# Optimization experiments

Hardware: AMD Instinct MI355X
Metric: run time of the kernel (lower is better)

The kernel has to match this reference:

```python
import jax, jax.numpy as jnp
from jax import lax
import numpy as np

WIN = 9  # default window [9, 9] in the original module


def _box_sum(x, win):
    """Sum over a win x win window, stride 1, pad win//2 (same as conv2d with ones kernel).
    Implemented separably (two 1D convs) - mathematically identical to the 2D ones-kernel conv.
    x: [B, 1, H, W] float32.
    """
    pad = win // 2
    kh = jnp.ones((1, 1, win, 1), x.dtype)
    kw = jnp.ones((1, 1, 1, win), x.dtype)
    dn = lax.conv_dimension_numbers(x.shape, kh.shape, ('NCHW', 'OIHW', 'NCHW'))
    y = lax.conv_general_dilated(x, kh, (1, 1), [(pad, pad), (0, 0)], dimension_numbers=dn)
    return lax.conv_general_dilated(y, kw, (1, 1), [(0, 0), (pad, pad)], dimension_numbers=dn)


def setup_inputs() -> dict:
    key = jax.random.key(0)
    k1, k2 = jax.random.split(key)
    shape = (32, 1, 512, 512)
    predict = jax.random.uniform(k1, shape, dtype=jnp.float32)
    target = jax.random.uniform(k2, shape, dtype=jnp.float32)
    return {"predict": predict, "target": target}


def reference(predict, target):
    win = WIN
    win_size = jnp.asarray(win * win, jnp.float32)

    I, J = predict, target
    I_sum = _box_sum(I, win)
    J_sum = _box_sum(J, win)
    I2_sum = _box_sum(I * I, win)
    J2_sum = _box_sum(J * J, win)
    IJ_sum = _box_sum(I * J, win)

    u_I = I_sum / win_size
    u_J = J_sum / win_size

    cross = IJ_sum - u_J * I_sum - u_I * J_sum + u_I * u_J * win_size
    I_var = I2_sum - 2.0 * u_I * I_sum + u_I * u_I * win_size
    J_var = J2_sum - 2.0 * u_J * J_sum + u_J * u_J * win_size

    cc = cross * cross / (I_var * J_var + 1e-6)
    return -jnp.mean(cc) + 1.0
```

## Files before the change

### kernel.cpp

```cpp
#include <hip/hip_runtime.h>


#define W 512
#define H 512
#define BH 16
#define NBANDS (H / BH)
#define NTHREADS 128

__device__ __forceinline__ float4 ld4(const float* p) {
    return *reinterpret_cast<const float4*>(p);
}

template<bool ADD>
__device__ __forceinline__ void row_accum(const float* __restrict__ Ip,
                                          const float* __restrict__ Jp,
                                          int rowbase, int x0,
                                          float vs[5][4]) {
    const float4 zz = make_float4(0.f, 0.f, 0.f, 0.f);
    float4 a0 = (x0 >= 4)     ? ld4(Ip + rowbase + x0 - 4) : zz;
    float4 a1 =                 ld4(Ip + rowbase + x0);
    float4 a2 = (x0 <= W - 8) ? ld4(Ip + rowbase + x0 + 4) : zz;
    float4 b0 = (x0 >= 4)     ? ld4(Jp + rowbase + x0 - 4) : zz;
    float4 b1 =                 ld4(Jp + rowbase + x0);
    float4 b2 = (x0 <= W - 8) ? ld4(Jp + rowbase + x0 + 4) : zz;

    float iv[12], jv[12];
    iv[0]=a0.x; iv[1]=a0.y; iv[2]=a0.z; iv[3]=a0.w;
    iv[4]=a1.x; iv[5]=a1.y; iv[6]=a1.z; iv[7]=a1.w;
    iv[8]=a2.x; iv[9]=a2.y; iv[10]=a2.z; iv[11]=a2.w;
    jv[0]=b0.x; jv[1]=b0.y; jv[2]=b0.z; jv[3]=b0.w;
    jv[4]=b1.x; jv[5]=b1.y; jv[6]=b1.z; jv[7]=b1.w;
    jv[8]=b2.x; jv[9]=b2.y; jv[10]=b2.z; jv[11]=b2.w;

    auto doq = [&](int qi, auto f) {
        float p[12];
        #pragma unroll
        for (int k = 0; k < 12; ++k) p[k] = f(k);
        float t = p[0];
        #pragma unroll
        for (int k = 1; k < 9; ++k) t += p[k];
        if (ADD) vs[qi][0] += t; else vs[qi][0] -= t;
        #pragma unroll
        for (int c = 1; c < 4; ++c) {
            t += p[c + 8] - p[c - 1];
            if (ADD) vs[qi][c] += t; else vs[qi][c] -= t;
        }
    };
    doq(0, [&](int k) { return iv[k]; });
    doq(1, [&](int k) { return jv[k]; });
    doq(2, [&](int k) { return iv[k] * iv[k]; });
    doq(3, [&](int k) { return jv[k] * jv[k]; });
    doq(4, [&](int k) { return iv[k] * jv[k]; });
}

__global__ __launch_bounds__(NTHREADS)
void ncc_main(const float* __restrict__ I, const float* __restrict__ J,
              float* __restrict__ partials) {
    const int blk  = blockIdx.x;
    const int b    = blk / NBANDS;
    const int band = blk % NBANDS;
    const int y0   = band * BH;
    const float* Ip = I + (size_t)b * (H * W);
    const float* Jp = J + (size_t)b * (H * W);
    const int x0 = (int)threadIdx.x * 4;

    float vs[5][4];
    #pragma unroll
    for (int q = 0; q < 5; ++q)
        #pragma unroll
        for (int c = 0; c < 4; ++c) vs[q][c] = 0.f;

    #pragma unroll
    for (int dr = -4; dr < 4; ++dr) {
        int r = y0 + dr;
        if (r >= 0 && r < H) row_accum<true>(Ip, Jp, r * W, x0, vs);
    }

    float cc_acc = 0.f;
    const float inv81 = 1.f / 81.f;
    for (int y = y0; y < y0 + BH; ++y) {
        int ra = y + 4;
        if (ra < H) row_accum<true>(Ip, Jp, ra * W, x0, vs);
        #pragma unroll
        for (int c = 0; c < 4; ++c) {
            float Is = vs[0][c], Js = vs[1][c];
            float I2 = vs[2][c], J2 = vs[3][c], IJ = vs[4][c];
            float cross = IJ - Is * Js * inv81;
            float Ivar  = I2 - Is * Is * inv81;
            float Jvar  = J2 - Js * Js * inv81;
            cc_acc += cross * cross / (Ivar * Jvar + 1e-6f);
        }
        int rs = y - 4;
        if (rs >= 0) row_accum<false>(Ip, Jp, rs * W, x0, vs);
    }

    #pragma unroll
    for (int off = 32; off > 0; off >>= 1)
        cc_acc += __shfl_down(cc_acc, off, 64);
    __shared__ float wsum[NTHREADS / 64];
    if ((threadIdx.x & 63) == 0) wsum[threadIdx.x >> 6] = cc_acc;
    __syncthreads();
    if (threadIdx.x == 0) partials[blockIdx.x] = wsum[0] + wsum[1];
}

__global__ __launch_bounds__(256)
void ncc_finish(const float* __restrict__ partials, float* __restrict__ out,
                int n, float inv_total) {
    float v = 0.f;
    for (int i = threadIdx.x; i < n; i += blockDim.x) v += partials[i];
    #pragma unroll
    for (int off = 32; off > 0; off >>= 1)
        v += __shfl_down(v, off, 64);
    __shared__ float wsum[4];
    if ((threadIdx.x & 63) == 0) wsum[threadIdx.x >> 6] = v;
    __syncthreads();
    if (threadIdx.x == 0) {
        float t = wsum[0] + wsum[1] + wsum[2] + wsum[3];
        out[0] = 1.0f - t * inv_total;
    }
}

extern "C" void kernel_launch(void* const* d_in, const int* in_sizes, int n_in,
                              void* d_out, int out_size, void* d_ws, size_t ws_size,
                              hipStream_t stream) {
    const float* I = (const float*)d_in[0];
    const float* J = (const float*)d_in[1];
    float* out = (float*)d_out;
    float* partials = (float*)d_ws;

    const int n = in_sizes[0];
    const int B = n / (H * W);
    const int nblocks = B * NBANDS;

    ncc_main<<<nblocks, NTHREADS, 0, stream>>>(I, J, partials);
    ncc_finish<<<1, 256, 0, stream>>>(partials, out, nblocks, 1.0f / (float)n);
}
```

Baseline: 119.6 us.

## Rewrite NCC kernel with register row ring, wave shuffles for horizontal sums

Each thread now owns two columns with 256 threads per block. It keeps a register ring of prefetched row pairs and does the vertical running sum first, then forms horizontal 9-wide sums through cross-lane shuffles, with wave-edge halos exchanged via double-buffered shared memory. Blocks are remapped with an XCD-style swizzle, and division is replaced by a hardware reciprocal. This removes the redundant 12-wide horizontal loads and the per-row recomputation. In exchange it adds a block barrier per row pair, shared-memory traffic and approximate reciprocal precision.

```diff
diff --git a/kernel.cpp b/kernel.cpp
--- a/kernel.cpp
+++ b/kernel.cpp
@@ -5,102 +5,161 @@
 #define H 512
 #define BH 16
 #define NBANDS (H / BH)
-#define NTHREADS 128
+#define NT 256
 
-__device__ __forceinline__ float4 ld4(const float* p) {
-    return *reinterpret_cast<const float4*>(p);
-}
-
-template<bool ADD>
-__device__ __forceinline__ void row_accum(const float* __restrict__ Ip,
-                                          const float* __restrict__ Jp,
-                                          int rowbase, int x0,
-                                          float vs[5][4]) {
-    const float4 zz = make_float4(0.f, 0.f, 0.f, 0.f);
-    float4 a0 = (x0 >= 4)     ? ld4(Ip + rowbase + x0 - 4) : zz;
-    float4 a1 =                 ld4(Ip + rowbase + x0);
-    float4 a2 = (x0 <= W - 8) ? ld4(Ip + rowbase + x0 + 4) : zz;
-    float4 b0 = (x0 >= 4)     ? ld4(Jp + rowbase + x0 - 4) : zz;
-    float4 b1 =                 ld4(Jp + rowbase + x0);
-    float4 b2 = (x0 <= W - 8) ? ld4(Jp + rowbase + x0 + 4) : zz;
-
-    float iv[12], jv[12];
-    iv[0]=a0.x; iv[1]=a0.y; iv[2]=a0.z; iv[3]=a0.w;
-    iv[4]=a1.x; iv[5]=a1.y; iv[6]=a1.z; iv[7]=a1.w;
-    iv[8]=a2.x; iv[9]=a2.y; iv[10]=a2.z; iv[11]=a2.w;
-    jv[0]=b0.x; jv[1]=b0.y; jv[2]=b0.z; jv[3]=b0.w;
-    jv[4]=b1.x; jv[5]=b1.y; jv[6]=b1.z; jv[7]=b1.w;
-    jv[8]=b2.x; jv[9]=b2.y; jv[10]=b2.z; jv[11]=b2.w;
-
-    auto doq = [&](int qi, auto f) {
-        float p[12];
-        #pragma unroll
-        for (int k = 0; k < 12; ++k) p[k] = f(k);
-        float t = p[0];
-        #pragma unroll
-        for (int k = 1; k < 9; ++k) t += p[k];
-        if (ADD) vs[qi][0] += t; else vs[qi][0] -= t;
-        #pragma unroll
-        for (int c = 1; c < 4; ++c) {
-            t += p[c + 8] - p[c - 1];
-            if (ADD) vs[qi][c] += t; else vs[qi][c] -= t;
-        }
-    };
-    doq(0, [&](int k) { return iv[k]; });
-    doq(1, [&](int k) { return jv[k]; });
-    doq(2, [&](int k) { return iv[k] * iv[k]; });
-    doq(3, [&](int k) { return jv[k] * jv[k]; });
-    doq(4, [&](int k) { return iv[k] * jv[k]; });
-}
-
-__global__ __launch_bounds__(NTHREADS)
+__global__ __launch_bounds__(NT)
 void ncc_main(const float* __restrict__ I, const float* __restrict__ J,
               float* __restrict__ partials) {
-    const int blk  = blockIdx.x;
-    const int b    = blk / NBANDS;
-    const int band = blk % NBANDS;
+    __shared__ float eb[2][2][6][4][5][3];
+    __shared__ float wsum[4];
+
+    const int tid  = threadIdx.x;
+    const int lane = tid & 63;
+    const int wid  = tid >> 6;
+
+    const int nblk = gridDim.x;
+    const int g    = (blockIdx.x & 7) * (nblk >> 3) + (blockIdx.x >> 3);
+
+    const int b    = g >> 5;
+    const int band = g & (NBANDS - 1);
     const int y0   = band * BH;
     const float* Ip = I + (size_t)b * (H * W);
     const float* Jp = J + (size_t)b * (H * W);
-    const int x0 = (int)threadIdx.x * 4;
+    const int c0 = tid * 2;
 
-    float vs[5][4];
+    for (int i = tid; i < 2 * 2 * 6 * 4 * 5 * 3; i += NT)
+        (&eb[0][0][0][0][0][0])[i] = 0.f;
+    __syncthreads();
+
+    float rg[7][8];
+    float v[5][2];
     #pragma unroll
-    for (int q = 0; q < 5; ++q)
-        #pragma unroll
-        for (int c = 0; c < 4; ++c) vs[q][c] = 0.f;
-
-    #pragma unroll
-    for (int dr = -4; dr < 4; ++dr) {
-        int r = y0 + dr;
-        if (r >= 0 && r < H) row_accum<true>(Ip, Jp, r * W, x0, vs);
-    }
+    for (int q = 0; q < 5; ++q) { v[q][0] = 0.f; v[q][1] = 0.f; }
 
     float cc_acc = 0.f;
     const float inv81 = 1.f / 81.f;
-    for (int y = y0; y < y0 + BH; ++y) {
-        int ra = y + 4;
-        if (ra < H) row_accum<true>(Ip, Jp, ra * W, x0, vs);
-        #pragma unroll
-        for (int c = 0; c < 4; ++c) {
-            float Is = vs[0][c], Js = vs[1][c];
-            float I2 = vs[2][c], J2 = vs[3][c], IJ = vs[4][c];
-            float cross = IJ - Is * Js * inv81;
-            float Ivar  = I2 - Is * Is * inv81;
-            float Jvar  = J2 - Js * Js * inv81;
-            cc_acc += cross * cross / (Ivar * Jvar + 1e-6f);
+
+    float a0[5], a1[5], b0[5], b1[5];
+
+    #pragma unroll
+    for (int t = 0; t < 14; ++t) {
+        if (t <= 11) {
+            const int gg = t % 7;
+            int r0 = y0 - 4 + 2 * t;
+            int rc0 = r0 < 0 ? 0 : (r0 > H - 1 ? H - 1 : r0);
+            int r1 = r0 + 1;
+            int rc1 = r1 < 0 ? 0 : (r1 > H - 1 ? H - 1 : r1);
+            float2 iA = *(const float2*)(Ip + rc0 * W + c0);
+            float2 jA = *(const float2*)(Jp + rc0 * W + c0);
+            float2 iB = *(const float2*)(Ip + rc1 * W + c0);
+            float2 jB = *(const float2*)(Jp + rc1 * W + c0);
+            rg[gg][0] = iA.x; rg[gg][1] = iA.y; rg[gg][2] = jA.x; rg[gg][3] = jA.y;
+            rg[gg][4] = iB.x; rg[gg][5] = iB.y; rg[gg][6] = jB.x; rg[gg][7] = jB.y;
         }
-        int rs = y - 4;
-        if (rs >= 0) row_accum<false>(Ip, Jp, rs * W, x0, vs);
+
+        #define MSK(k) ((y0 - 4 + (k)) >= 0 && (y0 - 4 + (k)) < H ? 1.f : 0.f)
+
+        #define VOP(gg, off, m, OP) do {                                      \
+            float _i0 = rg[gg][(off)+0], _i1 = rg[gg][(off)+1];               \
+            float _j0 = rg[gg][(off)+2], _j1 = rg[gg][(off)+3];               \
+            float _mi0 = (m) * _i0, _mi1 = (m) * _i1;                         \
+            float _mj0 = (m) * _j0, _mj1 = (m) * _j1;                         \
+            v[0][0] OP _mi0;        v[0][1] OP _mi1;                          \
+            v[1][0] OP _mj0;        v[1][1] OP _mj1;                          \
+            v[2][0] OP _mi0 * _i0;  v[2][1] OP _mi1 * _i1;                    \
+            v[3][0] OP _mj0 * _j0;  v[3][1] OP _mj1 * _j1;                    \
+            v[4][0] OP _mi0 * _j0;  v[4][1] OP _mi1 * _j1;                    \
+        } while (0)
+
+        if (t >= 2) { float m = MSK(2 * t - 4); VOP((t - 2) % 7, 0, m, +=); }
+        if (t >= 6) {
+            #pragma unroll
+            for (int q = 0; q < 5; ++q) { a0[q] = v[q][0]; a1[q] = v[q][1]; }
+            float m = MSK(2 * t - 12); VOP((t - 6) % 7, 0, m, -=);
+        }
+        if (t >= 2) { float m = MSK(2 * t - 3); VOP((t - 2) % 7, 4, m, +=); }
+        if (t >= 6) {
+            #pragma unroll
+            for (int q = 0; q < 5; ++q) { b0[q] = v[q][0]; b1[q] = v[q][1]; }
+            float m = MSK(2 * t - 11); VOP((t - 6) % 7, 4, m, -=);
+
+            const int par = t & 1;
+            const int cls = lane == 0 ? 0 : lane == 1 ? 1 :
+                            lane == 62 ? 2 : lane == 63 ? 3 : -1;
+            if (cls >= 0) {
+                #pragma unroll
+                for (int q = 0; q < 5; ++q) {
+                    eb[par][0][wid + 1][cls][q][0] = a0[q] + a1[q];
+                    eb[par][0][wid + 1][cls][q][1] = a0[q];
+                    eb[par][0][wid + 1][cls][q][2] = a1[q];
+                    eb[par][1][wid + 1][cls][q][0] = b0[q] + b1[q];
+                    eb[par][1][wid + 1][cls][q][1] = b0[q];
+                    eb[par][1][wid + 1][cls][q][2] = b1[q];
+                }
+            }
+            __syncthreads();
+
+            #define HROW(x0a, x1a, ab) do {                                   \
+                float h0[5], h1[5];                                           \
+                _Pragma("unroll")                                             \
+                for (int q = 0; q < 5; ++q) {                                 \
+                    float S    = x0a[q] + x1a[q];                             \
+                    float Sm2  = __shfl_up(S, 2);                             \
+                    float Sm1  = __shfl_up(S, 1);                             \
+                    float v0m2 = __shfl_up(x0a[q], 2);                        \
+                    float Sp1  = __shfl_down(S, 1);                           \
+                    float v0p2 = __shfl_down(x0a[q], 2);                      \
+                    float v1p2 = __shfl_down(x1a[q], 2);                      \
+                    if (lane == 0) {                                          \
+                        Sm2  = eb[par][ab][wid][2][q][0];                     \
+                        Sm1  = eb[par][ab][wid][3][q][0];                     \
+                        v0m2 = eb[par][ab][wid][2][q][1];                     \
+                    } else if (lane == 1) {                                   \
+                        Sm2  = eb[par][ab][wid][3][q][0];                     \
+                        v0m2 = eb[par][ab][wid][3][q][1];                     \
+                    }                                                         \
+                    if (lane == 63) {                                         \
+                        Sp1  = eb[par][ab][wid + 2][0][q][0];                 \
+                        v0p2 = eb[par][ab][wid + 2][1][q][1];                 \
+                        v1p2 = eb[par][ab][wid + 2][1][q][2];                 \
+                    } else if (lane == 62) {                                  \
+                        v0p2 = eb[par][ab][wid + 2][0][q][1];                 \
+                        v1p2 = eb[par][ab][wid + 2][0][q][2];                 \
+                    }                                                         \
+                    float t9 = ((Sm2 + Sm1) + (S + Sp1)) + v0p2;              \
+                    h0[q] = t9;                                               \
+                    h1[q] = (t9 - v0m2) + v1p2;                               \
+                }                                                             \
+                {                                                             \
+                    float Is = h0[0], Js = h0[1];                             \
+                    float u  = Is * inv81;                                    \
+                    float cr = h0[4] - u * Js;                                \
+                    float Iv = h0[2] - u * Is;                                \
+                    float Jv = h0[3] - (Js * inv81) * Js;                     \
+                    cc_acc += cr * cr * __builtin_amdgcn_rcpf(Iv * Jv + 1e-6f); \
+                }                                                             \
+                {                                                             \
+                    float Is = h1[0], Js = h1[1];                             \
+                    float u  = Is * inv81;                                    \
+                    float cr = h1[4] - u * Js;                                \
+                    float Iv = h1[2] - u * Is;                                \
+                    float Jv = h1[3] - (Js * inv81) * Js;                     \
+                    cc_acc += cr * cr * __builtin_amdgcn_rcpf(Iv * Jv + 1e-6f); \
+                }                                                             \
+            } while (0)
+
+            HROW(a0, a1, 0);
+            HROW(b0, b1, 1);
+        }
     }
 
     #pragma unroll
     for (int off = 32; off > 0; off >>= 1)
         cc_acc += __shfl_down(cc_acc, off, 64);
-    __shared__ float wsum[NTHREADS / 64];
-    if ((threadIdx.x & 63) == 0) wsum[threadIdx.x >> 6] = cc_acc;
+    if (lane == 0) wsum[wid] = cc_acc;
     __syncthreads();
-    if (threadIdx.x == 0) partials[blockIdx.x] = wsum[0] + wsum[1];
+    if (tid == 0)
+        partials[blockIdx.x] = (wsum[0] + wsum[1]) + (wsum[2] + wsum[3]);
 }
 
 __global__ __launch_bounds__(256)
@@ -115,7 +174,7 @@
     if ((threadIdx.x & 63) == 0) wsum[threadIdx.x >> 6] = v;
     __syncthreads();
     if (threadIdx.x == 0) {
-        float t = wsum[0] + wsum[1] + wsum[2] + wsum[3];
+        float t = (wsum[0] + wsum[1]) + (wsum[2] + wsum[3]);
         out[0] = 1.0f - t * inv_total;
     }
 }
@@ -132,6 +191,6 @@
     const int B = n / (H * W);
     const int nblocks = B * NBANDS;
 
-    ncc_main<<<nblocks, NTHREADS, 0, stream>>>(I, J, partials);
+    ncc_main<<<nblocks, NT, 0, stream>>>(I, J, partials);
     ncc_finish<<<1, 256, 0, stream>>>(partials, out, nblocks, 1.0f / (float)n);
 }
```

Measured after the change: 194.2 us. 62.4% more time.
